# Performance work log

Measured on AMD Instinct MI355X. Metric: run time of the kernel, lower is better.

## Reference

```python
import jax, jax.numpy as jnp
import numpy as np

N_HEAD, D_K, D_V, D_MODEL = 8, 64, 64, 512
LN_EPS = 1e-5

def setup_inputs() -> dict:
    key = jax.random.key(0)
    k1, k2, k3 = jax.random.split(key, 3)
    B, C, H, W = 8, D_MODEL, 32, 32
    q = jax.random.normal(k1, (B, C, H, W), dtype=jnp.float32)
    w_qkvs = jax.random.normal(k2, (N_HEAD * D_K, D_MODEL), dtype=jnp.float32) * np.sqrt(2.0 / (D_MODEL + D_K))
    fc_w = jax.random.normal(k3, (D_MODEL, N_HEAD * D_V), dtype=jnp.float32) * np.sqrt(2.0 / (N_HEAD * D_V + D_MODEL))
    fc_b = jnp.zeros((D_MODEL,), dtype=jnp.float32)
    ln_gamma = jnp.ones((D_MODEL,), dtype=jnp.float32)
    ln_beta = jnp.zeros((D_MODEL,), dtype=jnp.float32)
    return {"q": q, "w_qkvs": w_qkvs, "fc_w": fc_w, "fc_b": fc_b,
            "ln_gamma": ln_gamma, "ln_beta": ln_beta}

def reference(q, w_qkvs, fc_w, fc_b, ln_gamma, ln_beta):
    B, C, H, W = q.shape
    L = H * W
    temp = np.sqrt(D_K).astype(np.float32)
    # [B, C, H, W] -> [B, L, C] tokens
    x = q.reshape(B, C, L).transpose(0, 2, 1)
    residual = x
    # shared QKV projection -> per-head [B, h, L, d]
    qh = (x @ w_qkvs.T).reshape(B, L, N_HEAD, D_K).transpose(0, 2, 1, 3)
    # self-attention: q = k = v = qh
    scores = jnp.einsum('bhqd,bhkd->bhqk', qh, qh) / temp
    attn = jax.nn.softmax(scores, axis=-1)  # dropout is identity in eval
    out = jnp.einsum('bhqk,bhkd->bhqd', attn, qh)  # [B, h, L, d_v]
    # merge heads: [B, L, h*d_v]
    out = out.transpose(0, 2, 1, 3).reshape(B, L, N_HEAD * D_V)
    out = out @ fc_w.T + fc_b
    y = out + residual
    mu = jnp.mean(y, axis=-1, keepdims=True)
    var = jnp.mean(jnp.square(y - mu), axis=-1, keepdims=True)
    y = (y - mu) / jnp.sqrt(var + LN_EPS) * ln_gamma + ln_beta
    # raw reshape, matching torch .view(B, -1, H, W)
    return y.reshape(B, -1, H, W)
```

## Files before the change

kernel.cpp:

```cpp
#include <hip/hip_runtime.h>
#include <stdint.h>

#define BATCH 8
#define LTOK 1024
#define DMODEL 512
#define NHEAD 8
#define DHEAD 64

typedef unsigned short u16;
typedef u16 u16x8 __attribute__((ext_vector_type(8)));
typedef short bf16x8 __attribute__((ext_vector_type(8)));
typedef float f32x4 __attribute__((ext_vector_type(4)));

#define MFMA16(a,b,c) __builtin_amdgcn_mfma_f32_16x16x32_bf16((a),(b),(c),0,0,0)

__device__ __forceinline__ float bf2f(u16 x){
  union{unsigned u; float f;} v; v.u = ((unsigned)x)<<16; return v.f;
}
__device__ __forceinline__ u16 f2bf(float f){
  union{float f; unsigned u;} v; v.f = f;
  unsigned r = v.u + 0x7fffu + ((v.u>>16)&1u);
  return (u16)(r>>16);
}

__device__ __forceinline__ void gload_lds16(const u16* g, u16* l){
  __builtin_amdgcn_global_load_lds(
      (const __attribute__((address_space(1))) void*)g,
      (__attribute__((address_space(3))) void*)l,
      16, 0, 0);
}

__global__ __launch_bounds__(256) void convert_k(const float* __restrict__ src,
                                                 u16* __restrict__ dst, int n){
  const int i = (blockIdx.x*256 + threadIdx.x)*8;
  if (i >= n) return;
  u16x8 v;
  #pragma unroll
  for (int j=0;j<8;j++) v[j] = f2bf(src[i+j]);
  *(u16x8*)(dst + i) = v;
}

__global__ __launch_bounds__(256) void transpose_f2b(const float* __restrict__ src,
                                                     u16* __restrict__ dst,
                                                     int R, int C){
  __shared__ __align__(16) u16 t[64][72];
  const int b  = blockIdx.z;
  const int r0 = blockIdx.x*64, c0 = blockIdx.y*64;
  const float* s = src + (size_t)b*R*C;
  u16* d         = dst + (size_t)b*R*C;
  const int tid = threadIdx.x;
  const int row = tid>>3, ch = (tid&7)*8;
  #pragma unroll
  for (int rr=0; rr<64; rr+=32){
    const float* p = s + (size_t)(r0+row+rr)*C + c0 + ch;
    u16x8 v;
    #pragma unroll
    for (int j=0;j<8;j++) v[j] = f2bf(p[j]);
    *(u16x8*)&t[row+rr][ch] = v;
  }
  __syncthreads();
  #pragma unroll
  for (int rr=0; rr<64; rr+=32){
    const int dr = row+rr;
    u16x8 v;
    #pragma unroll
    for (int j=0;j<8;j++) v[j] = t[ch+j][dr];
    *(u16x8*)(d + (size_t)(c0+dr)*R + r0 + ch) = v;
  }
}

__device__ __forceinline__ void stage_gemm(const u16* __restrict__ src,
                                           int row0, int k0, u16* lds, int tid){
  #pragma unroll
  for (int s2=0; s2<2; ++s2){
    const int slot = tid + s2*256;
    const int row = slot>>3, ch8 = slot&7;
    const int k = k0 + ((ch8 ^ (row&7))<<3);
    gload_lds16(src + (size_t)(row0+row)*DMODEL + k, lds + slot*8);
  }
}

__global__ __launch_bounds__(256) void qkv_gemm(const u16* __restrict__ A,
                                                const u16* __restrict__ W,
                                                u16* __restrict__ Kf,
                                                u16* __restrict__ Vf){
  __shared__ __align__(128) u16 sA[2][4096];
  __shared__ __align__(128) u16 sB[2][4096];
  const int m0 = blockIdx.x*64, n0 = blockIdx.y*64;
  const int tid = threadIdx.x, w = tid>>6, lane = tid&63;
  const int wr = w>>1, wc = w&1;
  const int lr = lane&15, lg = lane>>4;
  f32x4 acc[2][2] = {};
  stage_gemm(A, m0, 0, sA[0], tid);
  stage_gemm(W, n0, 0, sB[0], tid);
  int buf = 0;
  for (int kt=0; kt<8; ++kt){
    __syncthreads();
    if (kt < 7){
      stage_gemm(A, m0, (kt+1)*64, sA[buf^1], tid);
      stage_gemm(W, n0, (kt+1)*64, sB[buf^1], tid);
    }
    #pragma unroll
    for (int ks=0; ks<2; ++ks){
      bf16x8 af[2], bfr[2];
      #pragma unroll
      for (int mi=0; mi<2; ++mi){
        const int r = wr*32 + mi*16 + lr;
        af[mi] = *(const bf16x8*)(&sA[buf][(r*64 + ks*32 + lg*8) ^ ((r&7)<<3)]);
      }
      #pragma unroll
      for (int nj=0; nj<2; ++nj){
        const int r = wc*32 + nj*16 + lr;
        bfr[nj] = *(const bf16x8*)(&sB[buf][(r*64 + ks*32 + lg*8) ^ ((r&7)<<3)]);
      }
      #pragma unroll
      for (int mi=0; mi<2; ++mi)
        #pragma unroll
        for (int nj=0; nj<2; ++nj)
          acc[mi][nj] = MFMA16(af[mi], bfr[nj], acc[mi][nj]);
    }
    buf ^= 1;
  }
  #pragma unroll
  for (int mi=0; mi<2; ++mi)
    #pragma unroll
    for (int nj=0; nj<2; ++nj)
      #pragma unroll
      for (int r=0; r<4; ++r){
        const int m = m0 + wr*32 + mi*16 + lg*4 + r;
        const int n = n0 + wc*32 + nj*16 + lr;
        const int bb = m>>10, l = m&1023, hh = n>>6, d = n&63;
        const int bh = bb*NHEAD + hh;
        const int t = l>>6;
        const u16 val = f2bf(acc[mi][nj][r]);
        {
          const int rr = l&63;
          const int fnj = rr>>4, flr = rr&15;
          const int fks = d>>5, flg = (d>>3)&3, fj = d&7;
          Kf[(size_t)(bh*16 + t)*4096 + (fks*4+fnj)*512 + (flg*16+flr)*8 + fj] = val;
        }
        {
          const int ll = l&63;
          const int fks = ll>>5, flg = (ll>>3)&3, fj = ll&7;
          const int fdj = d>>4, flr = d&15;
          Vf[(size_t)(bh*16 + t)*4096 + (fks*4+fdj)*512 + (flg*16+flr)*8 + fj] = val;
        }
      }
}

__global__ __launch_bounds__(256) void attn_k(const u16* __restrict__ kf,
                                              const u16* __restrict__ vf,
                                              u16* __restrict__ ao){
  __shared__ __align__(128) u16 sP[4096];
  const int bid = blockIdx.x;
  const int qt = bid >> 6, bh = bid & 63;
  const int b = bh >> 3, h = bh & 7;
  const u16* Kf = kf + (size_t)bh*16*4096;
  const u16* Vf = vf + (size_t)bh*16*4096;
  const int tid = threadIdx.x, w = tid>>6, lane = tid&63;
  const int lr = lane&15, lg = lane>>4;
  const int wp = w*1024;

  bf16x8 aq[2];
  #pragma unroll
  for (int ks=0; ks<2; ++ks){
    u16x8 v = *(const u16x8*)(Kf + (size_t)qt*4096 + (ks*4+w)*512 + lane*8);
    bf16x8 t;
    #pragma unroll
    for (int j=0;j<8;j++) t[j] = (short)f2bf(bf2f(v[j])*0.18033688f);
    aq[ks] = t;
  }

  f32x4 o[4] = {};
  float lsum[4] = {0.f,0.f,0.f,0.f};

  for (int kt=0; kt<16; ++kt){
    const u16* Kt = Kf + (size_t)kt*4096;
    const u16* Vt = Vf + (size_t)kt*4096;
    f32x4 sc[4] = {};
    __builtin_amdgcn_s_setprio(1);
    #pragma unroll
    for (int ks=0; ks<2; ++ks){
      #pragma unroll
      for (int nj=0; nj<4; ++nj){
        bf16x8 bk = *(const bf16x8*)(Kt + (ks*4+nj)*512 + lane*8);
        sc[nj] = MFMA16(aq[ks], bk, sc[nj]);
      }
    }
    __builtin_amdgcn_s_setprio(0);
    #pragma unroll
    for (int nj=0; nj<4; ++nj){
      #pragma unroll
      for (int r=0; r<4; ++r){
        const float p = __builtin_amdgcn_exp2f(sc[nj][r]);
        const unsigned pu = __float_as_uint(p) & 0xFFFF0000u;
        lsum[r] += __uint_as_float(pu);
        const int prow = lg*4 + r;
        sP[wp + ((prow*64 + nj*16 + lr) ^ ((prow&7)<<3))] = (u16)(pu>>16);
      }
    }
    asm volatile("s_waitcnt lgkmcnt(0)" ::: "memory");
    __builtin_amdgcn_s_setprio(1);
    #pragma unroll
    for (int ks=0; ks<2; ++ks){
      bf16x8 pa = *(const bf16x8*)(&sP[wp + ((lr*64 + ks*32 + lg*8) ^ ((lr&7)<<3))]);
      #pragma unroll
      for (int dj=0; dj<4; ++dj){
        bf16x8 bv = *(const bf16x8*)(Vt + (ks*4+dj)*512 + lane*8);
        o[dj] = MFMA16(pa, bv, o[dj]);
      }
    }
    __builtin_amdgcn_s_setprio(0);
  }

  float inv[4];
  #pragma unroll
  for (int r=0; r<4; ++r){
    float s = lsum[r];
    s += __shfl_xor(s,1); s += __shfl_xor(s,2);
    s += __shfl_xor(s,4); s += __shfl_xor(s,8);
    inv[r] = __builtin_amdgcn_rcpf(s);
  }
  const int i0 = qt*64 + w*16;
  #pragma unroll
  for (int dj=0; dj<4; ++dj)
    #pragma unroll
    for (int r=0; r<4; ++r){
      const int l = i0 + lg*4 + r;
      const int d = dj*16 + lr;
      ao[((size_t)(b*LTOK + l))*DMODEL + h*DHEAD + d] = f2bf(o[dj][r]*inv[r]);
    }
}

__global__ __launch_bounds__(256) void fc_gemm(const u16* __restrict__ A,
                                               const u16* __restrict__ W,
                                               const float* __restrict__ bias,
                                               const u16* __restrict__ resid,
                                               u16* __restrict__ Y){
  __shared__ __align__(128) u16 sA[2][4096];
  __shared__ __align__(128) u16 sB[2][4096];
  const int m0 = blockIdx.x*64, n0 = blockIdx.y*64;
  const int tid = threadIdx.x, w = tid>>6, lane = tid&63;
  const int wr = w>>1, wc = w&1;
  const int lr = lane&15, lg = lane>>4;
  f32x4 acc[2][2] = {};
  stage_gemm(A, m0, 0, sA[0], tid);
  stage_gemm(W, n0, 0, sB[0], tid);
  int buf = 0;
  for (int kt=0; kt<8; ++kt){
    __syncthreads();
    if (kt < 7){
      stage_gemm(A, m0, (kt+1)*64, sA[buf^1], tid);
      stage_gemm(W, n0, (kt+1)*64, sB[buf^1], tid);
    }
    #pragma unroll
    for (int ks=0; ks<2; ++ks){
      bf16x8 af[2], bfr[2];
      #pragma unroll
      for (int mi=0; mi<2; ++mi){
        const int r = wr*32 + mi*16 + lr;
        af[mi] = *(const bf16x8*)(&sA[buf][(r*64 + ks*32 + lg*8) ^ ((r&7)<<3)]);
      }
      #pragma unroll
      for (int nj=0; nj<2; ++nj){
        const int r = wc*32 + nj*16 + lr;
        bfr[nj] = *(const bf16x8*)(&sB[buf][(r*64 + ks*32 + lg*8) ^ ((r&7)<<3)]);
      }
      #pragma unroll
      for (int mi=0; mi<2; ++mi)
        #pragma unroll
        for (int nj=0; nj<2; ++nj)
          acc[mi][nj] = MFMA16(af[mi], bfr[nj], acc[mi][nj]);
    }
    buf ^= 1;
  }
  #pragma unroll
  for (int mi=0; mi<2; ++mi)
    #pragma unroll
    for (int nj=0; nj<2; ++nj)
      #pragma unroll
      for (int r=0; r<4; ++r){
        const int m = m0 + wr*32 + mi*16 + lg*4 + r;
        const int n = n0 + wc*32 + nj*16 + lr;
        const float val = acc[mi][nj][r] + bias[n] + bf2f(resid[(size_t)m*DMODEL+n]);
        Y[(size_t)m*DMODEL+n] = f2bf(val);
      }
}

__global__ __launch_bounds__(256) void ln_k(const u16* __restrict__ Y,
                                            const float* __restrict__ gamma,
                                            const float* __restrict__ beta,
                                            float* __restrict__ out){
  const int row = blockIdx.x*4 + (threadIdx.x>>6);
  const int lane = threadIdx.x&63;
  const u16* yr = Y + (size_t)row*DMODEL;
  u16x8 v = *(const u16x8*)(yr + lane*8);
  float x[8]; float s=0.f, sq=0.f;
  #pragma unroll
  for (int j=0;j<8;j++){ x[j]=bf2f(v[j]); s+=x[j]; sq+=x[j]*x[j]; }
  #pragma unroll
  for (int mk=1; mk<64; mk<<=1){ s += __shfl_xor(s,mk); sq += __shfl_xor(sq,mk); }
  const float mean = s*(1.f/DMODEL);
  float var = sq*(1.f/DMODEL) - mean*mean;
  const float rstd = rsqrtf(var + 1e-5f);
  float* po = out + (size_t)row*DMODEL + lane*8;
  #pragma unroll
  for (int j=0;j<8;j++){
    const int c = lane*8+j;
    po[j] = (x[j]-mean)*rstd*gamma[c] + beta[c];
  }
}

extern "C" void kernel_launch(void* const* d_in, const int* in_sizes, int n_in,
                              void* d_out, int out_size, void* d_ws, size_t ws_size,
                              hipStream_t stream){
  (void)in_sizes; (void)n_in; (void)out_size; (void)ws_size;
  const float* q      = (const float*)d_in[0];
  const float* w_qkvs = (const float*)d_in[1];
  const float* fc_w   = (const float*)d_in[2];
  const float* fc_b   = (const float*)d_in[3];
  const float* ln_g   = (const float*)d_in[4];
  const float* ln_b   = (const float*)d_in[5];
  float* out = (float*)d_out;
  char* ws = (char*)d_ws;
  u16* x_rm  = (u16*)(ws);
  u16* kfb   = (u16*)(ws + 8388608);
  u16* vfb   = (u16*)(ws + 16777216);
  u16* ao    = (u16*)(ws + 25165824);
  u16* wqkvb = (u16*)(ws + 33554432);
  u16* wfcb  = (u16*)(ws + 34078720);
  u16* y0    = kfb;

  convert_k<<<128,256,0,stream>>>(w_qkvs, wqkvb, DMODEL*DMODEL);
  convert_k<<<128,256,0,stream>>>(fc_w,   wfcb,  DMODEL*DMODEL);
  transpose_f2b<<<dim3(8,16,BATCH),256,0,stream>>>(q, x_rm, DMODEL, LTOK);
  qkv_gemm<<<dim3(128,8),256,0,stream>>>(x_rm, wqkvb, kfb, vfb);
  attn_k<<<1024,256,0,stream>>>(kfb, vfb, ao);
  fc_gemm<<<dim3(128,8),256,0,stream>>>(ao, wfcb, fc_b, x_rm, y0);
  ln_k<<<2048,256,0,stream>>>(y0, ln_g, ln_b, out);
}
```

Measured before the change: 85.98 us.

## Give each attention wave four query tiles to reuse K/V fragments

The attention kernel now has each wave process four 16-row query groups instead of one. K and V fragments are loaded into registers once per key tile and reused across all four groups, cutting global/L2 traffic for K and V by four. The grid shrinks from 1024 to 256 blocks, LDS for P grows fourfold, and launch bounds allow one block per CU. The trade-off is lower occupancy with only four waves per CU, which leaves less room to hide load and exp latency, plus higher register pressure.

```diff
diff --git a/kernel.cpp b/kernel.cpp
--- a/kernel.cpp
+++ b/kernel.cpp
@@ -148,10 +148,10 @@
       }
 }
 
-__global__ __launch_bounds__(256) void attn_k(const u16* __restrict__ kf,
-                                              const u16* __restrict__ vf,
-                                              u16* __restrict__ ao){
-  __shared__ __align__(128) u16 sP[4096];
+__global__ __launch_bounds__(256,1) void attn_k(const u16* __restrict__ kf,
+                                                const u16* __restrict__ vf,
+                                                u16* __restrict__ ao){
+  __shared__ __align__(128) u16 sP[16384];
   const int bid = blockIdx.x;
   const int qt = bid >> 6, bh = bid & 63;
   const int b = bh >> 3, h = bh & 7;
@@ -159,77 +159,97 @@
   const u16* Vf = vf + (size_t)bh*16*4096;
   const int tid = threadIdx.x, w = tid>>6, lane = tid&63;
   const int lr = lane&15, lg = lane>>4;
-  const int wp = w*1024;
-
-  bf16x8 aq[2];
-  #pragma unroll
-  for (int ks=0; ks<2; ++ks){
-    u16x8 v = *(const u16x8*)(Kf + (size_t)qt*4096 + (ks*4+w)*512 + lane*8);
-    bf16x8 t;
-    #pragma unroll
-    for (int j=0;j<8;j++) t[j] = (short)f2bf(bf2f(v[j])*0.18033688f);
-    aq[ks] = t;
-  }
-
-  f32x4 o[4] = {};
-  float lsum[4] = {0.f,0.f,0.f,0.f};
+  const int qtw = qt*4 + w;
+
+  bf16x8 aq[4][2];
+  #pragma unroll
+  for (int g=0; g<4; ++g)
+    #pragma unroll
+    for (int ks=0; ks<2; ++ks){
+      u16x8 v = *(const u16x8*)(Kf + (size_t)qtw*4096 + (ks*4+g)*512 + lane*8);
+      bf16x8 t;
+      #pragma unroll
+      for (int j=0;j<8;j++) t[j] = (short)f2bf(bf2f(v[j])*0.18033688f);
+      aq[g][ks] = t;
+    }
+
+  f32x4 o[4][4] = {};
+  float lsum[4][4] = {};
 
   for (int kt=0; kt<16; ++kt){
     const u16* Kt = Kf + (size_t)kt*4096;
     const u16* Vt = Vf + (size_t)kt*4096;
-    f32x4 sc[4] = {};
+    bf16x8 bk[2][4];
+    #pragma unroll
+    for (int ks=0; ks<2; ++ks)
+      #pragma unroll
+      for (int nj=0; nj<4; ++nj)
+        bk[ks][nj] = *(const bf16x8*)(Kt + (ks*4+nj)*512 + lane*8);
+    #pragma unroll
+    for (int g=0; g<4; ++g){
+      f32x4 sc[4] = {};
+      __builtin_amdgcn_s_setprio(1);
+      #pragma unroll
+      for (int ks=0; ks<2; ++ks)
+        #pragma unroll
+        for (int nj=0; nj<4; ++nj)
+          sc[nj] = MFMA16(aq[g][ks], bk[ks][nj], sc[nj]);
+      __builtin_amdgcn_s_setprio(0);
+      const int wp = (w*4+g)*1024;
+      #pragma unroll
+      for (int nj=0; nj<4; ++nj){
+        #pragma unroll
+        for (int r=0; r<4; ++r){
+          const float p = __builtin_amdgcn_exp2f(sc[nj][r]);
+          const unsigned pu = __float_as_uint(p) & 0xFFFF0000u;
+          lsum[g][r] += __uint_as_float(pu);
+          const int prow = lg*4 + r;
+          sP[wp + ((prow*64 + nj*16 + lr) ^ ((prow&7)<<3))] = (u16)(pu>>16);
+        }
+      }
+    }
+    asm volatile("s_waitcnt lgkmcnt(0)" ::: "memory");
+    bf16x8 bv[2][4];
+    #pragma unroll
+    for (int ks=0; ks<2; ++ks)
+      #pragma unroll
+      for (int dj=0; dj<4; ++dj)
+        bv[ks][dj] = *(const bf16x8*)(Vt + (ks*4+dj)*512 + lane*8);
     __builtin_amdgcn_s_setprio(1);
     #pragma unroll
-    for (int ks=0; ks<2; ++ks){
-      #pragma unroll
-      for (int nj=0; nj<4; ++nj){
-        bf16x8 bk = *(const bf16x8*)(Kt + (ks*4+nj)*512 + lane*8);
-        sc[nj] = MFMA16(aq[ks], bk, sc[nj]);
+    for (int g=0; g<4; ++g){
+      const int wp = (w*4+g)*1024;
+      #pragma unroll
+      for (int ks=0; ks<2; ++ks){
+        bf16x8 pa = *(const bf16x8*)(&sP[wp + ((lr*64 + ks*32 + lg*8) ^ ((lr&7)<<3))]);
+        #pragma unroll
+        for (int dj=0; dj<4; ++dj)
+          o[g][dj] = MFMA16(pa, bv[ks][dj], o[g][dj]);
       }
     }
     __builtin_amdgcn_s_setprio(0);
-    #pragma unroll
-    for (int nj=0; nj<4; ++nj){
+  }
+
+  #pragma unroll
+  for (int g=0; g<4; ++g){
+    float inv[4];
+    #pragma unroll
+    for (int r=0; r<4; ++r){
+      float s = lsum[g][r];
+      s += __shfl_xor(s,1); s += __shfl_xor(s,2);
+      s += __shfl_xor(s,4); s += __shfl_xor(s,8);
+      inv[r] = __builtin_amdgcn_rcpf(s);
+    }
+    const int i0 = qtw*64 + g*16;
+    #pragma unroll
+    for (int dj=0; dj<4; ++dj)
       #pragma unroll
       for (int r=0; r<4; ++r){
-        const float p = __builtin_amdgcn_exp2f(sc[nj][r]);
-        const unsigned pu = __float_as_uint(p) & 0xFFFF0000u;
-        lsum[r] += __uint_as_float(pu);
-        const int prow = lg*4 + r;
-        sP[wp + ((prow*64 + nj*16 + lr) ^ ((prow&7)<<3))] = (u16)(pu>>16);
-      }
-    }
-    asm volatile("s_waitcnt lgkmcnt(0)" ::: "memory");
-    __builtin_amdgcn_s_setprio(1);
-    #pragma unroll
-    for (int ks=0; ks<2; ++ks){
-      bf16x8 pa = *(const bf16x8*)(&sP[wp + ((lr*64 + ks*32 + lg*8) ^ ((lr&7)<<3))]);
-      #pragma unroll
-      for (int dj=0; dj<4; ++dj){
-        bf16x8 bv = *(const bf16x8*)(Vt + (ks*4+dj)*512 + lane*8);
-        o[dj] = MFMA16(pa, bv, o[dj]);
-      }
-    }
-    __builtin_amdgcn_s_setprio(0);
-  }
-
-  float inv[4];
-  #pragma unroll
-  for (int r=0; r<4; ++r){
-    float s = lsum[r];
-    s += __shfl_xor(s,1); s += __shfl_xor(s,2);
-    s += __shfl_xor(s,4); s += __shfl_xor(s,8);
-    inv[r] = __builtin_amdgcn_rcpf(s);
-  }
-  const int i0 = qt*64 + w*16;
-  #pragma unroll
-  for (int dj=0; dj<4; ++dj)
-    #pragma unroll
-    for (int r=0; r<4; ++r){
-      const int l = i0 + lg*4 + r;
-      const int d = dj*16 + lr;
-      ao[((size_t)(b*LTOK + l))*DMODEL + h*DHEAD + d] = f2bf(o[dj][r]*inv[r]);
-    }
+        const int l = i0 + lg*4 + r;
+        const int d = dj*16 + lr;
+        ao[((size_t)(b*LTOK + l))*DMODEL + h*DHEAD + d] = f2bf(o[g][dj][r]*inv[r]);
+      }
+  }
 }
 
 __global__ __launch_bounds__(256) void fc_gemm(const u16* __restrict__ A,
@@ -335,7 +355,7 @@
   convert_k<<<128,256,0,stream>>>(fc_w,   wfcb,  DMODEL*DMODEL);
   transpose_f2b<<<dim3(8,16,BATCH),256,0,stream>>>(q, x_rm, DMODEL, LTOK);
   qkv_gemm<<<dim3(128,8),256,0,stream>>>(x_rm, wqkvb, kfb, vfb);
-  attn_k<<<1024,256,0,stream>>>(kfb, vfb, ao);
+  attn_k<<<256,256,0,stream>>>(kfb, vfb, ao);
   fc_gemm<<<dim3(128,8),256,0,stream>>>(ao, wfcb, fc_b, x_rm, y0);
   ln_k<<<2048,256,0,stream>>>(y0, ln_g, ln_b, out);
 }
```

After: 81.67 us. 5.0% less time.
